# Kernel optimization log

Measured on AMD Instinct MI355X. Metric: run time of the kernel, lower is better.

Reference implementation:

```python
import jax, jax.numpy as jnp
import numpy as np

N = 8192          # num_relations
IN_DIM = 512      # 2 * entity_dim
HID = 256         # hidden_dim
REL_DIM = 256     # relation_dim


def setup_inputs() -> dict:
    key = jax.random.key(0)
    ks = jax.random.split(key, 8)
    s = 1.0 / np.sqrt(IN_DIM)
    return {
        "relation": jax.random.normal(ks[0], (N, REL_DIM), dtype=jnp.float32),
        "context": jax.random.normal(ks[1], (N, IN_DIM), dtype=jnp.float32),
        "adj_tensor": jax.random.randint(ks[2], (N, N), 0, 2).astype(jnp.float32),
        "W_common": jax.random.normal(ks[3], (HID, IN_DIM), dtype=jnp.float32) * s,
        "w_left": jax.random.normal(ks[4], (HID,), dtype=jnp.float32) * (1.0 / np.sqrt(HID)),
        "b_left": jax.random.normal(ks[5], (), dtype=jnp.float32) * 0.01,
        "w_right": jax.random.normal(ks[6], (HID,), dtype=jnp.float32) * (1.0 / np.sqrt(HID)),
        "b_right": jax.random.normal(ks[7], (), dtype=jnp.float32) * 0.01,
    }


def reference(relation, context, adj_tensor, W_common, w_left, b_left, w_right, b_right):
    # common linear (no bias): (N, IN_DIM) @ (IN_DIM, HID) -> (N, HID)
    in_fts = context @ W_common.T
    left = in_fts @ w_left + b_left          # (N,)
    right = in_fts @ w_right + b_right       # (N,)
    logits = left[:, None] + right[None, :]  # additive outer-sum -> (N, N)
    logits = jnp.where(logits >= 0, logits, 0.2 * logits)  # leaky_relu(0.2)
    logits = jnp.where(adj_tensor <= 0.0, -jnp.inf, logits)
    coefs = jax.nn.softmax(logits, axis=-1)  # (N, N)
    x = coefs @ relation                     # (N, REL_DIM)
    return jax.nn.relu(x)
```

## Files before the change

kernel.cpp:

```cpp
#include <hip/hip_runtime.h>

#define NREL 8192
#define RD   256

typedef float f32x4 __attribute__((ext_vector_type(4)));
typedef short s16x8 __attribute__((ext_vector_type(8)));
typedef unsigned int  u32;
typedef unsigned short u16;
typedef unsigned long long u64;
typedef u32 u32x4 __attribute__((ext_vector_type(4)));

__device__ __forceinline__ u16 f2bf(float f) {
    u32 b = __float_as_uint(f);
    return (u16)((b + 0x7FFFu + ((b >> 16) & 1u)) >> 16);
}
__device__ __forceinline__ u32 pk_bf16(float lo, float hi) {
    u32 r;
    asm("v_cvt_pk_bf16_f32 %0, %1, %2" : "=v"(r) : "v"(lo), "v"(hi));
    return r;
}

__global__ __launch_bounds__(256) void k_prep_bf(
    const float* __restrict__ W, const float* __restrict__ wl,
    const float* __restrict__ wr, float* __restrict__ ul,
    float* __restrict__ ur, const float* __restrict__ R,
    u32* __restrict__ Bf)
{
    __shared__ float sL[256], sR[256];
    const int t = threadIdx.x;
    if (blockIdx.x < 32) {
        const int d = blockIdx.x * 16 + (t & 15);
        float aL = 0.f, aR = 0.f;
        for (int h = (t >> 4); h < 256; h += 16) {
            float w = W[h * 512 + d];
            aL += w * wl[h];
            aR += w * wr[h];
        }
        sL[t] = aL; sR[t] = aR;
        __syncthreads();
        if (t < 16) {
            float xL = 0.f, xR = 0.f;
            for (int g = 0; g < 16; g++) { xL += sL[g * 16 + t]; xR += sR[g * 16 + t]; }
            ul[blockIdx.x * 16 + t] = xL;
            ur[blockIdx.x * 16 + t] = xR;
        }
        return;
    }
    if (!Bf) return;
    const int b     = blockIdx.x - 32;
    const int jt    = b >> 1;
    const int fbase = (b & 1) * 1024;
    #pragma unroll
    for (int rep = 0; rep < 4; rep++) {
        const int f    = fbase + rep * 256 + t;
        const int kk   = f >> 10;
        const int cg   = (f >> 6) & 15;
        const int lane = f & 63;
        const int lq   = lane >> 4;
        const int l15  = lane & 15;
        const int j0   = (jt << 6) + kk * 32 + lq * 8;
        const int n    = cg * 16 + l15;
        const float* src = R + (size_t)j0 * RD + n;
        float v[8];
        #pragma unroll
        for (int e = 0; e < 8; e++) v[e] = src[(size_t)e * RD];
        u32x4 w;
        w.x = pk_bf16(v[0], v[1]);
        w.y = pk_bf16(v[2], v[3]);
        w.z = pk_bf16(v[4], v[5]);
        w.w = pk_bf16(v[6], v[7]);
        *(u32x4*)(Bf + ((size_t)jt * 2048 + f) * 4) = w;
    }
}

__global__ __launch_bounds__(256) void k_lr(
    const float* __restrict__ ctx, const float* __restrict__ ul,
    const float* __restrict__ ur, const float* __restrict__ bl,
    const float* __restrict__ br, float* __restrict__ left,
    float* __restrict__ right)
{
    const int lane = threadIdx.x & 63;
    const int row  = blockIdx.x * 4 + (threadIdx.x >> 6);
    const f32x4* cv = (const f32x4*)(ctx + (size_t)row * 512);
    const f32x4* uv = (const f32x4*)ul;
    const f32x4* vv = (const f32x4*)ur;
    f32x4 c0 = cv[lane], c1 = cv[lane + 64];
    f32x4 u0 = uv[lane], u1 = uv[lane + 64];
    f32x4 v0 = vv[lane], v1 = vv[lane + 64];
    float dl = c0.x*u0.x + c0.y*u0.y + c0.z*u0.z + c0.w*u0.w
             + c1.x*u1.x + c1.y*u1.y + c1.z*u1.z + c1.w*u1.w;
    float dr = c0.x*v0.x + c0.y*v0.y + c0.z*v0.z + c0.w*v0.w
             + c1.x*v1.x + c1.y*v1.y + c1.z*v1.z + c1.w*v1.w;
    #pragma unroll
    for (int o = 1; o < 64; o <<= 1) { dl += __shfl_xor(dl, o); dr += __shfl_xor(dr, o); }
    if (lane == 0) {
        left[row]  = dl + bl[0];
        right[row] = dr + br[0];
    }
}

__global__ __launch_bounds__(256) void k_rmax(const float* __restrict__ right,
                                              u32* __restrict__ rmaxk)
{
    __shared__ float sm[4];
    const int t = threadIdx.x;
    const f32x4* rv = (const f32x4*)right;
    float m = -3.4e38f;
    #pragma unroll
    for (int i = 0; i < 8; i++) {
        f32x4 v = rv[t + 256 * i];
        m = fmaxf(m, fmaxf(fmaxf(v.x, v.y), fmaxf(v.z, v.w)));
    }
    #pragma unroll
    for (int o = 1; o < 64; o <<= 1) m = fmaxf(m, __shfl_xor(m, o));
    if ((t & 63) == 0) sm[t >> 6] = m;
    __syncthreads();
    if (t == 0) {
        m = fmaxf(fmaxf(sm[0], sm[1]), fmaxf(sm[2], sm[3]));
        u32 b = __float_as_uint(m);
        *rmaxk = ((int)b >= 0) ? (b | 0x80000000u) : ~b;
    }
}

template<int S>
__global__ __launch_bounds__(512) void k_attn_f(
    const float* __restrict__ adj, const s16x8* __restrict__ Bf,
    const float* __restrict__ left, const float* __restrict__ right,
    const u32* __restrict__ rmaxk, float* __restrict__ pnum,
    float* __restrict__ pden)
{
    __shared__ u32 Pl[2][2048];

    const int tid  = threadIdx.x;
    const int lane = tid & 63;
    const int wv   = tid >> 6;
    const int l15  = lane & 15;
    const int lq   = lane >> 4;
    const int s      = (int)(blockIdx.x % (unsigned)S);
    const int rowblk = (int)(blockIdx.x / (unsigned)S) * 64;
    const int jt0 = s * (128 / S);
    const int jt1 = jt0 + (128 / S);

    const int pr = tid >> 4;
    const int pq = tid & 15;

    const float lft0 = left[rowblk + pr];
    const float lft1 = left[rowblk + pr + 32];
    const u32 kbits = *rmaxk;
    const float rmax = __uint_as_float((kbits & 0x80000000u) ? (kbits ^ 0x80000000u)
                                                             : ~kbits);
    float z;
    z = lft0 + rmax; const float m0 = fmaxf(z, 0.2f * z);
    z = lft1 + rmax; const float m1 = fmaxf(z, 0.2f * z);

    f32x4 acc[4][2];
    #pragma unroll
    for (int i = 0; i < 4; i++) { acc[i][0] = (f32x4)0.f; acc[i][1] = (f32x4)0.f; }
    float dp0 = 0.f, dp1 = 0.f;

    const f32x4* adjv = (const f32x4*)adj;
    const f32x4* rv4  = (const f32x4*)right;
    const size_t arow0 = (size_t)(rowblk + pr) * 2048;
    const size_t arow1 = (size_t)(rowblk + pr + 32) * 2048;

    const u32 widx0 = (u32)pr * 32 + (((u32)pq * 2) ^ (((u32)pr & 7) << 2));
    const u32 widx1 = widx0 + 1024;

    f32x4 aA0 = adjv[arow0 + jt0 * 16 + pq];
    f32x4 aA1 = adjv[arow1 + jt0 * 16 + pq];
    f32x4 rvA = rv4[jt0 * 16 + pq];
    f32x4 aB0 = adjv[arow0 + (jt0 + 1) * 16 + pq];
    f32x4 aB1 = adjv[arow1 + (jt0 + 1) * 16 + pq];
    f32x4 rvB = rv4[(jt0 + 1) * 16 + pq];
    s16x8 bA[2][2], bB[2][2];
    #pragma unroll
    for (int kk = 0; kk < 2; kk++)
        #pragma unroll
        for (int ct = 0; ct < 2; ct++)
            bA[kk][ct] = Bf[(size_t)jt0 * 2048 + kk * 1024 + (wv * 2 + ct) * 64 + lane];

    for (int jt = jt0; jt < jt1; jt += 2) {
        {
            float pa[4], pb[4];
            #pragma unroll
            for (int e = 0; e < 4; e++) {
                const float r = rvA[e];
                float z0 = lft0 + r; float s0 = fmaxf(z0, 0.2f * z0);
                float e0 = __expf(s0 - m0);
                pa[e] = (aA0[e] > 0.5f) ? e0 : 0.f;
                float z1 = lft1 + r; float s1 = fmaxf(z1, 0.2f * z1);
                float e1 = __expf(s1 - m1);
                pb[e] = (aA1[e] > 0.5f) ? e1 : 0.f;
            }
            dp0 += pa[0] + pa[1] + pa[2] + pa[3];
            dp1 += pb[0] + pb[1] + pb[2] + pb[3];
            Pl[0][widx0]     = pk_bf16(pa[0], pa[1]);
            Pl[0][widx0 + 1] = pk_bf16(pa[2], pa[3]);
            Pl[0][widx1]     = pk_bf16(pb[0], pb[1]);
            Pl[0][widx1 + 1] = pk_bf16(pb[2], pb[3]);

            asm volatile("s_waitcnt lgkmcnt(0)" ::: "memory");
            __builtin_amdgcn_s_barrier();

            const int j2 = (jt + 2 < jt1) ? jt + 2 : jt0;
            aA0 = adjv[arow0 + j2 * 16 + pq];
            aA1 = adjv[arow1 + j2 * 16 + pq];
            rvA = rv4[j2 * 16 + pq];
            #pragma unroll
            for (int kk = 0; kk < 2; kk++)
                #pragma unroll
                for (int ct = 0; ct < 2; ct++)
                    bB[kk][ct] = Bf[(size_t)(jt + 1) * 2048 + kk * 1024
                                    + (wv * 2 + ct) * 64 + lane];

            const u16* Pu = (const u16*)Pl[0];
            #pragma unroll
            for (int kk = 0; kk < 2; kk++) {
                s16x8 af[4];
                #pragma unroll
                for (int rt = 0; rt < 4; rt++) {
                    const int row = rt * 16 + l15;
                    const int us  = row * 64 + ((kk * 32 + lq * 8) ^ ((row & 7) << 3));
                    af[rt] = *(const s16x8*)(Pu + us);
                }
                #pragma unroll
                for (int ct = 0; ct < 2; ct++)
                    #pragma unroll
                    for (int rt = 0; rt < 4; rt++)
                        acc[rt][ct] = __builtin_amdgcn_mfma_f32_16x16x32_bf16(
                            af[rt], bA[kk][ct], acc[rt][ct], 0, 0, 0);
            }
        }
        {
            float pa[4], pb[4];
            #pragma unroll
            for (int e = 0; e < 4; e++) {
                const float r = rvB[e];
                float z0 = lft0 + r; float s0 = fmaxf(z0, 0.2f * z0);
                float e0 = __expf(s0 - m0);
                pa[e] = (aB0[e] > 0.5f) ? e0 : 0.f;
                float z1 = lft1 + r; float s1 = fmaxf(z1, 0.2f * z1);
                float e1 = __expf(s1 - m1);
                pb[e] = (aB1[e] > 0.5f) ? e1 : 0.f;
            }
            dp0 += pa[0] + pa[1] + pa[2] + pa[3];
            dp1 += pb[0] + pb[1] + pb[2] + pb[3];
            Pl[1][widx0]     = pk_bf16(pa[0], pa[1]);
            Pl[1][widx0 + 1] = pk_bf16(pa[2], pa[3]);
            Pl[1][widx1]     = pk_bf16(pb[0], pb[1]);
            Pl[1][widx1 + 1] = pk_bf16(pb[2], pb[3]);

            asm volatile("s_waitcnt lgkmcnt(0)" ::: "memory");
            __builtin_amdgcn_s_barrier();

            const int j3 = (jt + 3 < jt1) ? jt + 3 : jt0;
            aB0 = adjv[arow0 + j3 * 16 + pq];
            aB1 = adjv[arow1 + j3 * 16 + pq];
            rvB = rv4[j3 * 16 + pq];
            const int j2 = (jt + 2 < jt1) ? jt + 2 : jt0;
            #pragma unroll
            for (int kk = 0; kk < 2; kk++)
                #pragma unroll
                for (int ct = 0; ct < 2; ct++)
                    bA[kk][ct] = Bf[(size_t)j2 * 2048 + kk * 1024
                                    + (wv * 2 + ct) * 64 + lane];

            const u16* Pu = (const u16*)Pl[1];
            #pragma unroll
            for (int kk = 0; kk < 2; kk++) {
                s16x8 af[4];
                #pragma unroll
                for (int rt = 0; rt < 4; rt++) {
                    const int row = rt * 16 + l15;
                    const int us  = row * 64 + ((kk * 32 + lq * 8) ^ ((row & 7) << 3));
                    af[rt] = *(const s16x8*)(Pu + us);
                }
                #pragma unroll
                for (int ct = 0; ct < 2; ct++)
                    #pragma unroll
                    for (int rt = 0; rt < 4; rt++)
                        acc[rt][ct] = __builtin_amdgcn_mfma_f32_16x16x32_bf16(
                            af[rt], bB[kk][ct], acc[rt][ct], 0, 0, 0);
            }
        }
    }

    #pragma unroll
    for (int o = 1; o < 16; o <<= 1) { dp0 += __shfl_xor(dp0, o); dp1 += __shfl_xor(dp1, o); }
    if (pq == 0) {
        pden[(size_t)s * NREL + rowblk + pr]      = dp0;
        pden[(size_t)s * NREL + rowblk + pr + 32] = dp1;
    }
    float* pn = pnum + (size_t)s * NREL * RD;
    #pragma unroll
    for (int rt = 0; rt < 4; rt++)
        #pragma unroll
        for (int ct = 0; ct < 2; ct++)
            #pragma unroll
            for (int r = 0; r < 4; r++) {
                const int row = rt * 16 + lq * 4 + r;
                pn[(size_t)(rowblk + row) * RD + (wv * 32 + ct * 16 + l15)] =
                    acc[rt][ct][r];
            }
}

template<int S>
__global__ __launch_bounds__(256) void k_red(
    const float* __restrict__ pnum, const float* __restrict__ pden,
    float* __restrict__ out)
{
    const int idx = blockIdx.x * 256 + threadIdx.x;
    const int row = idx >> 6;
    float den = 0.f;
    #pragma unroll
    for (int s = 0; s < S; s++) den += pden[(size_t)s * NREL + row];
    const f32x4* pn4 = (const f32x4*)pnum;
    f32x4 a = (f32x4)0.f;
    #pragma unroll
    for (int s = 0; s < S; s++) a += pn4[(size_t)s * (NREL * RD / 4) + idx];
    f32x4 r;
    r.x = fmaxf(a.x / den, 0.f);
    r.y = fmaxf(a.y / den, 0.f);
    r.z = fmaxf(a.z / den, 0.f);
    r.w = fmaxf(a.w / den, 0.f);
    ((f32x4*)out)[idx] = r;
}

__global__ __launch_bounds__(512) void k_attn_leg(
    const float* __restrict__ adj, const float* __restrict__ rel,
    const float* __restrict__ left, const float* __restrict__ right,
    const u32* __restrict__ rmaxk, float* __restrict__ outp)
{
    __shared__ u32   Pl[64 * 32];
    __shared__ float dnm[64];
    const int tid  = threadIdx.x;
    const int lane = tid & 63;
    const int wv   = tid >> 6;
    const int l15  = lane & 15;
    const int lq   = lane >> 4;
    const int rowblk = blockIdx.x * 64;
    const int pr = tid >> 4, pq = tid & 15;
    const float lft0 = left[rowblk + pr];
    const float lft1 = left[rowblk + pr + 32];
    const u32 kbits = *rmaxk;
    const float rmax = __uint_as_float((kbits & 0x80000000u) ? (kbits ^ 0x80000000u)
                                                             : ~kbits);
    float z;
    z = lft0 + rmax; const float m0 = fmaxf(z, 0.2f * z);
    z = lft1 + rmax; const float m1 = fmaxf(z, 0.2f * z);
    f32x4 acc[4][2];
    #pragma unroll
    for (int i = 0; i < 4; i++) { acc[i][0] = (f32x4)0.f; acc[i][1] = (f32x4)0.f; }
    float dp0 = 0.f, dp1 = 0.f;
    const f32x4* adjv = (const f32x4*)adj;
    const f32x4* rv4  = (const f32x4*)right;
    const size_t arow0 = (size_t)(rowblk + pr) * 2048;
    const size_t arow1 = (size_t)(rowblk + pr + 32) * 2048;
    const int n0 = wv * 32 + l15;
    const u32 widx0 = (u32)pr * 32 + (((u32)pq * 2) ^ (((u32)pr & 7) << 2));
    const u32 widx1 = widx0 + 1024;
    for (int jb = 0; jb < NREL; jb += 64) {
        f32x4 a0 = adjv[arow0 + (jb >> 2) + pq];
        f32x4 a1 = adjv[arow1 + (jb >> 2) + pq];
        f32x4 rv = rv4[(jb >> 2) + pq];
        s16x8 bc[2][2];
        #pragma unroll
        for (int kk = 0; kk < 2; kk++)
            #pragma unroll
            for (int ct = 0; ct < 2; ct++) {
                const float* rp = rel + (size_t)(jb + kk * 32 + lq * 8) * RD
                                      + (n0 + ct * 16);
                s16x8 b;
                #pragma unroll
                for (int e = 0; e < 8; e++) b[e] = (short)f2bf(rp[(size_t)e * RD]);
                bc[kk][ct] = b;
            }
        float pa[4], pb[4];
        #pragma unroll
        for (int e = 0; e < 4; e++) {
            const float r = rv[e];
            float z0 = lft0 + r; float s0 = fmaxf(z0, 0.2f * z0);
            pa[e] = a0[e] * __expf(s0 - m0);
            float z1 = lft1 + r; float s1 = fmaxf(z1, 0.2f * z1);
            pb[e] = a1[e] * __expf(s1 - m1);
        }
        dp0 += pa[0] + pa[1] + pa[2] + pa[3];
        dp1 += pb[0] + pb[1] + pb[2] + pb[3];
        Pl[widx0]     = pk_bf16(pa[0], pa[1]);
        Pl[widx0 + 1] = pk_bf16(pa[2], pa[3]);
        Pl[widx1]     = pk_bf16(pb[0], pb[1]);
        Pl[widx1 + 1] = pk_bf16(pb[2], pb[3]);
        __syncthreads();
        #pragma unroll
        for (int kk = 0; kk < 2; kk++) {
            s16x8 af[4];
            #pragma unroll
            for (int rt = 0; rt < 4; rt++) {
                const int row = rt * 16 + l15;
                const int us  = row * 64 + ((kk * 32 + lq * 8) ^ ((row & 7) << 3));
                af[rt] = *(const s16x8*)((const u16*)Pl + us);
            }
            #pragma unroll
            for (int ct = 0; ct < 2; ct++)
                #pragma unroll
                for (int rt = 0; rt < 4; rt++)
                    acc[rt][ct] = __builtin_amdgcn_mfma_f32_16x16x32_bf16(
                        af[rt], bc[kk][ct], acc[rt][ct], 0, 0, 0);
        }
        __syncthreads();
    }
    #pragma unroll
    for (int o = 1; o < 16; o <<= 1) { dp0 += __shfl_xor(dp0, o); dp1 += __shfl_xor(dp1, o); }
    if (pq == 0) { dnm[pr] = dp0; dnm[pr + 32] = dp1; }
    __syncthreads();
    #pragma unroll
    for (int rt = 0; rt < 4; rt++)
        #pragma unroll
        for (int ct = 0; ct < 2; ct++)
            #pragma unroll
            for (int r = 0; r < 4; r++) {
                const int row = rt * 16 + lq * 4 + r;
                float v = acc[rt][ct][r] / dnm[row];
                outp[(size_t)(rowblk + row) * RD + (wv * 32 + ct * 16 + l15)] =
                    fmaxf(v, 0.f);
            }
}

extern "C" void kernel_launch(void* const* d_in, const int* in_sizes, int n_in,
                              void* d_out, int out_size, void* d_ws, size_t ws_size,
                              hipStream_t stream)
{
    const float* relation = (const float*)d_in[0];
    const float* context  = (const float*)d_in[1];
    const float* adj      = (const float*)d_in[2];
    const float* W        = (const float*)d_in[3];
    const float* wl       = (const float*)d_in[4];
    const float* bl       = (const float*)d_in[5];
    const float* wr       = (const float*)d_in[6];
    const float* br       = (const float*)d_in[7];
    float* out = (float*)d_out;

    float* wsf   = (float*)d_ws;
    float* ul    = wsf;
    float* ur    = wsf + 512;
    float* left  = wsf + 1024;
    float* right = wsf + 1024 + 8192;
    u32*   rmaxk = (u32*)(wsf + 1024 + 16384);
    const size_t hdr  = 81920;
    const size_t bf_b = (size_t)NREL * RD * 2;
    u32* Bf   = (u32*)((char*)d_ws + hdr);
    float* pnum = (float*)((char*)d_ws + hdr + bf_b);

    const int S = 4;
    const size_t need = hdr + bf_b
                      + (size_t)S * NREL * RD * 4 + (size_t)S * NREL * 4;

    if (ws_size >= need) {
        float* pden = pnum + (size_t)S * NREL * RD;
        hipLaunchKernelGGL(k_prep_bf, dim3(288), dim3(256), 0, stream,
                           W, wl, wr, ul, ur, relation, Bf);
        hipLaunchKernelGGL(k_lr, dim3(2048), dim3(256), 0, stream,
                           context, ul, ur, bl, br, left, right);
        hipLaunchKernelGGL(k_rmax, dim3(1), dim3(256), 0, stream, right, rmaxk);
        hipLaunchKernelGGL((k_attn_f<4>), dim3(128 * 4), dim3(512), 0, stream,
                           adj, (const s16x8*)Bf, left, right, rmaxk, pnum, pden);
        hipLaunchKernelGGL((k_red<4>), dim3(2048), dim3(256), 0, stream,
                           pnum, pden, out);
    } else {
        hipLaunchKernelGGL(k_prep_bf, dim3(32), dim3(256), 0, stream,
                           W, wl, wr, ul, ur, relation, (u32*)nullptr);
        hipLaunchKernelGGL(k_lr, dim3(2048), dim3(256), 0, stream,
                           context, ul, ur, bl, br, left, right);
        hipLaunchKernelGGL(k_rmax, dim3(1), dim3(256), 0, stream, right, rmaxk);
        hipLaunchKernelGGL(k_attn_leg, dim3(128), dim3(512), 0, stream,
                           adj, relation, left, right, rmaxk, out);
    }
}
```

Measured before the change: 109.0 us.

## Double row tile to 128 with 1024-thread blocks, nontemporal adj loads

Doubles the attention kernel's row block from 64 to 128 rows per workgroup using 1024 threads (16 waves split into two row groups of eight column waves), so each fetched B-fragment of relation serves twice as many rows. Adjacency loads become nontemporal to avoid polluting cache with the streamed 256MB matrix, and the mask select is replaced by multiplying the exp by the adjacency value. The grid halves to 256 blocks, which lowers parallelism and raises per-block LDS and register pressure. The multiply-based mask assumes adjacency entries are exactly 0 or 1.

```diff
diff --git a/kernel.cpp b/kernel.cpp
--- a/kernel.cpp
+++ b/kernel.cpp
@@ -18,6 +18,9 @@
     u32 r;
     asm("v_cvt_pk_bf16_f32 %0, %1, %2" : "=v"(r) : "v"(lo), "v"(hi));
     return r;
+}
+__device__ __forceinline__ f32x4 ntload(const f32x4* p) {
+    return __builtin_nontemporal_load(p);
 }
 
 __global__ __launch_bounds__(256) void k_prep_bf(
@@ -123,21 +126,23 @@
 }
 
 template<int S>
-__global__ __launch_bounds__(512) void k_attn_f(
+__global__ __launch_bounds__(1024) void k_attn_f(
     const float* __restrict__ adj, const s16x8* __restrict__ Bf,
     const float* __restrict__ left, const float* __restrict__ right,
     const u32* __restrict__ rmaxk, float* __restrict__ pnum,
     float* __restrict__ pden)
 {
-    __shared__ u32 Pl[2][2048];
+    __shared__ u32 Pl[2][4096];
 
     const int tid  = threadIdx.x;
     const int lane = tid & 63;
     const int wv   = tid >> 6;
     const int l15  = lane & 15;
     const int lq   = lane >> 4;
+    const int rg   = wv >> 3;
+    const int cg8  = wv & 7;
     const int s      = (int)(blockIdx.x % (unsigned)S);
-    const int rowblk = (int)(blockIdx.x / (unsigned)S) * 64;
+    const int rowblk = (int)(blockIdx.x / (unsigned)S) * 128;
     const int jt0 = s * (128 / S);
     const int jt1 = jt0 + (128 / S);
 
@@ -145,7 +150,7 @@
     const int pq = tid & 15;
 
     const float lft0 = left[rowblk + pr];
-    const float lft1 = left[rowblk + pr + 32];
+    const float lft1 = left[rowblk + pr + 64];
     const u32 kbits = *rmaxk;
     const float rmax = __uint_as_float((kbits & 0x80000000u) ? (kbits ^ 0x80000000u)
                                                              : ~kbits);
@@ -161,23 +166,23 @@
     const f32x4* adjv = (const f32x4*)adj;
     const f32x4* rv4  = (const f32x4*)right;
     const size_t arow0 = (size_t)(rowblk + pr) * 2048;
-    const size_t arow1 = (size_t)(rowblk + pr + 32) * 2048;
+    const size_t arow1 = (size_t)(rowblk + pr + 64) * 2048;
 
     const u32 widx0 = (u32)pr * 32 + (((u32)pq * 2) ^ (((u32)pr & 7) << 2));
-    const u32 widx1 = widx0 + 1024;
-
-    f32x4 aA0 = adjv[arow0 + jt0 * 16 + pq];
-    f32x4 aA1 = adjv[arow1 + jt0 * 16 + pq];
+    const u32 widx1 = widx0 + 2048;
+
+    f32x4 aA0 = ntload(&adjv[arow0 + jt0 * 16 + pq]);
+    f32x4 aA1 = ntload(&adjv[arow1 + jt0 * 16 + pq]);
     f32x4 rvA = rv4[jt0 * 16 + pq];
-    f32x4 aB0 = adjv[arow0 + (jt0 + 1) * 16 + pq];
-    f32x4 aB1 = adjv[arow1 + (jt0 + 1) * 16 + pq];
+    f32x4 aB0 = ntload(&adjv[arow0 + (jt0 + 1) * 16 + pq]);
+    f32x4 aB1 = ntload(&adjv[arow1 + (jt0 + 1) * 16 + pq]);
     f32x4 rvB = rv4[(jt0 + 1) * 16 + pq];
     s16x8 bA[2][2], bB[2][2];
     #pragma unroll
     for (int kk = 0; kk < 2; kk++)
         #pragma unroll
         for (int ct = 0; ct < 2; ct++)
-            bA[kk][ct] = Bf[(size_t)jt0 * 2048 + kk * 1024 + (wv * 2 + ct) * 64 + lane];
+            bA[kk][ct] = Bf[(size_t)jt0 * 2048 + kk * 1024 + (cg8 * 2 + ct) * 64 + lane];
 
     for (int jt = jt0; jt < jt1; jt += 2) {
         {
@@ -186,11 +191,9 @@
             for (int e = 0; e < 4; e++) {
                 const float r = rvA[e];
                 float z0 = lft0 + r; float s0 = fmaxf(z0, 0.2f * z0);
-                float e0 = __expf(s0 - m0);
-                pa[e] = (aA0[e] > 0.5f) ? e0 : 0.f;
+                pa[e] = aA0[e] * __expf(s0 - m0);
                 float z1 = lft1 + r; float s1 = fmaxf(z1, 0.2f * z1);
-                float e1 = __expf(s1 - m1);
-                pb[e] = (aA1[e] > 0.5f) ? e1 : 0.f;
+                pb[e] = aA1[e] * __expf(s1 - m1);
             }
             dp0 += pa[0] + pa[1] + pa[2] + pa[3];
             dp1 += pb[0] + pb[1] + pb[2] + pb[3];
@@ -203,15 +206,15 @@
             __builtin_amdgcn_s_barrier();
 
             const int j2 = (jt + 2 < jt1) ? jt + 2 : jt0;
-            aA0 = adjv[arow0 + j2 * 16 + pq];
-            aA1 = adjv[arow1 + j2 * 16 + pq];
+            aA0 = ntload(&adjv[arow0 + j2 * 16 + pq]);
+            aA1 = ntload(&adjv[arow1 + j2 * 16 + pq]);
             rvA = rv4[j2 * 16 + pq];
             #pragma unroll
             for (int kk = 0; kk < 2; kk++)
                 #pragma unroll
                 for (int ct = 0; ct < 2; ct++)
                     bB[kk][ct] = Bf[(size_t)(jt + 1) * 2048 + kk * 1024
-                                    + (wv * 2 + ct) * 64 + lane];
+                                    + (cg8 * 2 + ct) * 64 + lane];
 
             const u16* Pu = (const u16*)Pl[0];
             #pragma unroll
@@ -219,7 +222,7 @@
                 s16x8 af[4];
                 #pragma unroll
                 for (int rt = 0; rt < 4; rt++) {
-                    const int row = rt * 16 + l15;
+                    const int row = rg * 64 + rt * 16 + l15;
                     const int us  = row * 64 + ((kk * 32 + lq * 8) ^ ((row & 7) << 3));
                     af[rt] = *(const s16x8*)(Pu + us);
                 }
@@ -237,11 +240,9 @@
             for (int e = 0; e < 4; e++) {
                 const float r = rvB[e];
                 float z0 = lft0 + r; float s0 = fmaxf(z0, 0.2f * z0);
-                float e0 = __expf(s0 - m0);
-                pa[e] = (aB0[e] > 0.5f) ? e0 : 0.f;
+                pa[e] = aB0[e] * __expf(s0 - m0);
                 float z1 = lft1 + r; float s1 = fmaxf(z1, 0.2f * z1);
-                float e1 = __expf(s1 - m1);
-                pb[e] = (aB1[e] > 0.5f) ? e1 : 0.f;
+                pb[e] = aB1[e] * __expf(s1 - m1);
             }
             dp0 += pa[0] + pa[1] + pa[2] + pa[3];
             dp1 += pb[0] + pb[1] + pb[2] + pb[3];
@@ -254,8 +255,8 @@
             __builtin_amdgcn_s_barrier();
 
             const int j3 = (jt + 3 < jt1) ? jt + 3 : jt0;
-            aB0 = adjv[arow0 + j3 * 16 + pq];
-            aB1 = adjv[arow1 + j3 * 16 + pq];
+            aB0 = ntload(&adjv[arow0 + j3 * 16 + pq]);
+            aB1 = ntload(&adjv[arow1 + j3 * 16 + pq]);
             rvB = rv4[j3 * 16 + pq];
             const int j2 = (jt + 2 < jt1) ? jt + 2 : jt0;
             #pragma unroll
@@ -263,7 +264,7 @@
                 #pragma unroll
                 for (int ct = 0; ct < 2; ct++)
                     bA[kk][ct] = Bf[(size_t)j2 * 2048 + kk * 1024
-                                    + (wv * 2 + ct) * 64 + lane];
+                                    + (cg8 * 2 + ct) * 64 + lane];
 
             const u16* Pu = (const u16*)Pl[1];
             #pragma unroll
@@ -271,7 +272,7 @@
                 s16x8 af[4];
                 #pragma unroll
                 for (int rt = 0; rt < 4; rt++) {
-                    const int row = rt * 16 + l15;
+                    const int row = rg * 64 + rt * 16 + l15;
                     const int us  = row * 64 + ((kk * 32 + lq * 8) ^ ((row & 7) << 3));
                     af[rt] = *(const s16x8*)(Pu + us);
                 }
@@ -289,7 +290,7 @@
     for (int o = 1; o < 16; o <<= 1) { dp0 += __shfl_xor(dp0, o); dp1 += __shfl_xor(dp1, o); }
     if (pq == 0) {
         pden[(size_t)s * NREL + rowblk + pr]      = dp0;
-        pden[(size_t)s * NREL + rowblk + pr + 32] = dp1;
+        pden[(size_t)s * NREL + rowblk + pr + 64] = dp1;
     }
     float* pn = pnum + (size_t)s * NREL * RD;
     #pragma unroll
@@ -298,8 +299,8 @@
         for (int ct = 0; ct < 2; ct++)
             #pragma unroll
             for (int r = 0; r < 4; r++) {
-                const int row = rt * 16 + lq * 4 + r;
-                pn[(size_t)(rowblk + row) * RD + (wv * 32 + ct * 16 + l15)] =
+                const int row = rg * 64 + rt * 16 + lq * 4 + r;
+                pn[(size_t)(rowblk + row) * RD + (cg8 * 32 + ct * 16 + l15)] =
                     acc[rt][ct][r];
             }
 }
@@ -462,7 +463,7 @@
         hipLaunchKernelGGL(k_lr, dim3(2048), dim3(256), 0, stream,
                            context, ul, ur, bl, br, left, right);
         hipLaunchKernelGGL(k_rmax, dim3(1), dim3(256), 0, stream, right, rmaxk);
-        hipLaunchKernelGGL((k_attn_f<4>), dim3(128 * 4), dim3(512), 0, stream,
+        hipLaunchKernelGGL((k_attn_f<4>), dim3(64 * 4), dim3(1024), 0, stream,
                            adj, (const s16x8*)Bf, left, right, rmaxk, pnum, pden);
         hipLaunchKernelGGL((k_red<4>), dim3(2048), dim3(256), 0, stream,
                            pnum, pden, out);
```

Measured after the change: 107.7 us. Within noise of the previous version (-1.2%).
